# Optimization experiments

Hardware: AMD Instinct MI355X
Metric: run time of the kernel (lower is better)

## Reference

```python
import jax, jax.numpy as jnp
import numpy as np

VOCAB_P1 = 100001  # vocab_size + 1
EMB_DIM = 128
BATCH = 256
NNZ_Q = 2048
NNZ_D = 262144


def setup_inputs() -> dict:
    key = jax.random.key(0)
    ks = jax.random.split(key, 10)
    return {
        "q_rows": jax.random.randint(ks[0], (NNZ_Q,), 0, VOCAB_P1, dtype=jnp.int32),
        "q_cols": jax.random.randint(ks[1], (NNZ_Q,), 0, BATCH, dtype=jnp.int32),
        "q_vals": jax.random.uniform(ks[2], (NNZ_Q,), dtype=jnp.float32),
        "d_rows": jax.random.randint(ks[3], (NNZ_D,), 0, VOCAB_P1, dtype=jnp.int32),
        "d_cols": jax.random.randint(ks[4], (NNZ_D,), 0, BATCH, dtype=jnp.int32),
        "d_freqs": jax.random.uniform(ks[5], (NNZ_D,), dtype=jnp.float32),
        "emb": jax.random.normal(ks[6], (VOCAB_P1, EMB_DIM), dtype=jnp.float32) * 0.1,
        "W1": jax.random.normal(ks[7], (EMB_DIM, 100), dtype=jnp.float32) * (2.0 / EMB_DIM) ** 0.5,
        "b1": jnp.zeros((100,), dtype=jnp.float32),
        "W2": jax.random.normal(ks[8], (100, 1), dtype=jnp.float32) * (2.0 / 100) ** 0.5,
        "b2": jnp.ones((1,), dtype=jnp.float32),
        "mu": jnp.float32(2500.0),
        "batch_size": BATCH,
    }


def _scatter_dense(rows, cols, vals, batch_size):
    # tf.sparse.to_dense: dense [vocab+1, batch] with values at (row, col).
    # Indices are (assumed) unique, so add == set; add keeps it a clean scatter.
    return jnp.zeros((VOCAB_P1, batch_size), vals.dtype).at[rows, cols].add(vals)


def reference(q_rows, q_cols, q_vals, d_rows, d_cols, d_freqs,
              emb, W1, b1, W2, b2, mu, batch_size):
    # query bag-of-words dense tensor [V, B]
    q = _scatter_dense(q_rows, q_cols, q_vals, batch_size)

    # term discrimination value MLP on document terms (dropout disabled = eval mode)
    h = jax.nn.relu(emb[d_rows] @ W1 + b1)          # [nnz_d, 100]
    tdv = jax.nn.relu(h @ W2 + b2)[:, 0]            # [nnz_d]
    freq_tdv = tdv * d_freqs                        # [nnz_d]

    # weighted document term-frequency dense tensor [V, B]
    d = _scatter_dense(d_rows, d_cols, freq_tdv, batch_size)

    cfreq = jnp.sum(d, axis=1) / jnp.sum(d)                     # [V]
    smoothing = jnp.log(mu / (jnp.sum(d, axis=0) + mu))         # [B]
    dir_d = jnp.log1p(d / (1.0 + mu * cfreq[:, None])) + smoothing  # [V, B]
    rel = jnp.sum(q * dir_d, axis=0)                            # [B]
    return (rel, d)
```

## Files before the change

### kernel.cpp

```cpp
#include <hip/hip_runtime.h>
#include <stdint.h>

#define VOCAB_P1 100001
#define EMB_DIM  128
#define BATCH    256
#define NNZ_Q    2048
#define NNZ_D    262144

#define NPAD 112
#define ROWP 136
#define NGRP 6251
#define MBLK 1563
#define BINBLK 512

#define NBKT 3126
#define BCAP 192
#define CSC  64

#define WS_BCNT  0
#define WS_CS    12544
#define WS_TDV   78080
#define WS_RSUM  478096
#define WS_W1BF  878112
#define WS_BIN   908576

typedef __attribute__((ext_vector_type(8))) short  short8;
typedef __attribute__((ext_vector_type(4))) float  float4v;

__device__ __forceinline__ unsigned short f2bf(float f) {
    union { float f; unsigned u; } v; v.f = f;
    unsigned u = v.u;
    u += 0x7fffu + ((u >> 16) & 1u);
    return (unsigned short)(u >> 16);
}

__device__ __forceinline__ short8 cvt8(float4 a, float4 b) {
    short8 r;
    r[0] = (short)f2bf(a.x); r[1] = (short)f2bf(a.y);
    r[2] = (short)f2bf(a.z); r[3] = (short)f2bf(a.w);
    r[4] = (short)f2bf(b.x); r[5] = (short)f2bf(b.y);
    r[6] = (short)f2bf(b.z); r[7] = (short)f2bf(b.w);
    return r;
}

__global__ __launch_bounds__(256) void prep_kernel(
    float* __restrict__ rel, int* __restrict__ wsbase,
    int* __restrict__ w1bfi, const float* __restrict__ W1)
{
    int t = blockIdx.x * 256 + threadIdx.x;
    const int4 z = {0, 0, 0, 0};
    if (t < 4880) ((int4*)wsbase)[t] = z;
    else if (t < 4944) ((int4*)rel)[t - 4880] = z;
    for (int i = t; i < (NPAD * ROWP) / 2; i += 6144) {
        int p0 = 2 * i, p1 = 2 * i + 1;
        int j0 = p0 / ROWP, k0 = p0 - j0 * ROWP;
        int j1 = p1 / ROWP, k1 = p1 - j1 * ROWP;
        unsigned lo = (j0 < 100 && k0 < 128) ? f2bf(W1[k0 * 100 + j0]) : 0u;
        unsigned hi = (j1 < 100 && k1 < 128) ? f2bf(W1[k1 * 100 + j1]) : 0u;
        w1bfi[i] = (int)(lo | (hi << 16));
    }
}

__global__ __launch_bounds__(256) void mlp_bin_kernel(
    const float* __restrict__ emb, const float* __restrict__ b1,
    const float* __restrict__ W2, const float* __restrict__ b2,
    const short* __restrict__ w1bf, float* __restrict__ tdvtab,
    const int* __restrict__ d_rows, const int* __restrict__ d_cols,
    const float* __restrict__ d_freqs,
    int* __restrict__ bcnt, int2* __restrict__ binbuf)
{
    const int tid = threadIdx.x;

    if (blockIdx.x >= MBLK) {
        int g = (blockIdx.x - MBLK) * 256 + tid;
        int2   r2 = ((const int2*)d_rows)[g];
        int2   c2 = ((const int2*)d_cols)[g];
        float2 f2 = ((const float2*)d_freqs)[g];
        int bk0 = r2.x >> 5, bk1 = r2.y >> 5;
        int i0 = atomicAdd(&bcnt[bk0], 1);
        int i1 = atomicAdd(&bcnt[bk1], 1);
        if (i0 < BCAP)
            binbuf[bk0 * BCAP + i0] = make_int2(((r2.x & 31) << 8) | c2.x,
                                                __float_as_int(f2.x));
        if (i1 < BCAP)
            binbuf[bk1 * BCAP + i1] = make_int2(((r2.y & 31) << 8) | c2.y,
                                                __float_as_int(f2.y));
        return;
    }

    __shared__ __align__(16) short w1t[NPAD * ROWP];
    __shared__ float b1s[NPAD];
    __shared__ float w2s[NPAD];

    {
        const int4* src = (const int4*)w1bf;
        int4* dst = (int4*)w1t;
        #pragma unroll
        for (int k = 0; k < 8; ++k) {
            int idx = tid + k * 256;
            if (idx < (NPAD * ROWP * 2) / 16) dst[idx] = src[idx];
        }
    }
    if (tid < NPAD) {
        b1s[tid] = (tid < 100) ? b1[tid] : 0.f;
        w2s[tid] = (tid < 100) ? W2[tid] : 0.f;
    }
    __syncthreads();

    const int lane = tid & 63;
    const int w    = tid >> 6;
    const int col  = lane & 15;
    const int quad = lane >> 4;
    const float b2v = b2[0];

    const int grp = blockIdx.x * 4 + w;
    if (grp >= NGRP) return;

    int r  = grp * 16 + col;
    int rr = (r <= VOCAB_P1 - 1) ? r : (VOCAB_P1 - 1);
    const float* rp = emb + (size_t)rr * EMB_DIM + quad * 8;
    float4 u0 = *(const float4*)(rp);
    float4 u1 = *(const float4*)(rp + 4);
    float4 u2 = *(const float4*)(rp + 32);
    float4 u3 = *(const float4*)(rp + 36);
    float4 u4 = *(const float4*)(rp + 64);
    float4 u5 = *(const float4*)(rp + 68);
    float4 u6 = *(const float4*)(rp + 96);
    float4 u7 = *(const float4*)(rp + 100);
    short8 a0 = cvt8(u0, u1), a1 = cvt8(u2, u3);
    short8 a2 = cvt8(u4, u5), a3 = cvt8(u6, u7);

    float s0 = 0.f, s1 = 0.f, s2 = 0.f, s3 = 0.f;
    for (int jt = 0; jt < 7; ++jt) {
        const short* bp = &w1t[(jt * 16 + col) * ROWP + quad * 8];
        short8 bv0 = *(const short8*)(bp);
        short8 bv1 = *(const short8*)(bp + 32);
        short8 bv2 = *(const short8*)(bp + 64);
        short8 bv3 = *(const short8*)(bp + 96);

        float4v acc = {0.f, 0.f, 0.f, 0.f};
        acc = __builtin_amdgcn_mfma_f32_16x16x32_bf16(a0, bv0, acc, 0, 0, 0);
        acc = __builtin_amdgcn_mfma_f32_16x16x32_bf16(a1, bv1, acc, 0, 0, 0);
        acc = __builtin_amdgcn_mfma_f32_16x16x32_bf16(a2, bv2, acc, 0, 0, 0);
        acc = __builtin_amdgcn_mfma_f32_16x16x32_bf16(a3, bv3, acc, 0, 0, 0);

        float b1v = b1s[jt * 16 + col];
        float w2v = w2s[jt * 16 + col];
        float h;
        h = acc[0] + b1v; h = h > 0.f ? h : 0.f; s0 += h * w2v;
        h = acc[1] + b1v; h = h > 0.f ? h : 0.f; s1 += h * w2v;
        h = acc[2] + b1v; h = h > 0.f ? h : 0.f; s2 += h * w2v;
        h = acc[3] + b1v; h = h > 0.f ? h : 0.f; s3 += h * w2v;
    }
    for (int m = 1; m < 16; m <<= 1) {
        s0 += __shfl_xor(s0, m, 64);
        s1 += __shfl_xor(s1, m, 64);
        s2 += __shfl_xor(s2, m, 64);
        s3 += __shfl_xor(s3, m, 64);
    }
    if (col < 4) {
        float sv = (col == 0) ? s0 : (col == 1) ? s1 : (col == 2) ? s2 : s3;
        int row = grp * 16 + quad * 4 + col;
        if (row < VOCAB_P1) {
            float tdv = sv + b2v;
            tdvtab[row] = tdv > 0.f ? tdv : 0.f;
        }
    }
}

__global__ __launch_bounds__(256) void compose_kernel(
    const int* __restrict__ bcnt, const int2* __restrict__ binbuf,
    const float* __restrict__ tdvtab, float* __restrict__ dmat,
    float* __restrict__ rowsum, float* __restrict__ colsum2)
{
    __shared__ float tile[32 * 256];
    const int tid = threadIdx.x;
    const int blk = blockIdx.x;

    const float4 z = {0.f, 0.f, 0.f, 0.f};
    float4* t4 = (float4*)tile;
    #pragma unroll
    for (int k = 0; k < 8; ++k) t4[tid + k * 256] = z;
    __syncthreads();

    const int row0 = blk * 32;
    int cnt = bcnt[blk]; if (cnt > BCAP) cnt = BCAP;
    for (int i = tid; i < cnt; i += 256) {
        int2 e = binbuf[blk * BCAP + i];
        int rl = e.x >> 8, c = e.x & 255;
        float v = __int_as_float(e.y) * tdvtab[row0 + rl];
        atomicAdd(&tile[rl * 256 + c], v);
    }
    __syncthreads();

    int vrows = VOCAB_P1 - row0; if (vrows > 32) vrows = 32;

    float4* out4 = (float4*)(dmat + (size_t)row0 * BATCH);
    const int lim = vrows * 64;
    #pragma unroll
    for (int k = 0; k < 8; ++k) {
        int idx = tid + k * 256;
        if (idx < lim) out4[idx] = t4[idx];
    }

    {
        int rl = tid >> 3, seg = tid & 7;
        float s = 0.f;
        #pragma unroll
        for (int j = 0; j < 32; ++j)
            s += tile[rl * 256 + seg * 32 + ((j + tid) & 31)];
        s += __shfl_xor(s, 1, 64);
        s += __shfl_xor(s, 2, 64);
        s += __shfl_xor(s, 4, 64);
        if (seg == 0 && rl < vrows) rowsum[row0 + rl] = s;
    }

    {
        float cs = 0.f;
        #pragma unroll
        for (int r = 0; r < 32; ++r) cs += tile[r * 256 + tid];
        atomicAdd(&colsum2[(blk & (CSC - 1)) * BATCH + tid], cs);
    }
}

__global__ __launch_bounds__(256) void relv2_kernel(
    const int* __restrict__ q_rows, const int* __restrict__ q_cols,
    const float* __restrict__ q_vals, const float* __restrict__ dmat,
    const float* __restrict__ rowsum, const float* __restrict__ colsum2,
    const float* __restrict__ mu_p, float* __restrict__ rel)
{
    __shared__ float csT[BATCH];
    __shared__ float tot4[4];
    const int tid = threadIdx.x;

    float s = 0.f;
    #pragma unroll 8
    for (int k = 0; k < CSC; ++k) s += colsum2[k * BATCH + tid];
    csT[tid] = s;
    float p = s;
    for (int m = 1; m < 64; m <<= 1) p += __shfl_xor(p, m, 64);
    if ((tid & 63) == 0) tot4[tid >> 6] = p;
    __syncthreads();
    float total = tot4[0] + tot4[1] + tot4[2] + tot4[3];

    int e = blockIdx.x * 256 + tid;
    int v = q_rows[e], b = q_cols[e];
    float qv = q_vals[e];
    float mu = mu_p[0];
    float dval = dmat[(size_t)v * BATCH + b];
    float cf   = rowsum[v] / total;
    float dir  = log1pf(dval / (1.f + mu * cf)) + logf(mu / (csT[b] + mu));
    atomicAdd(&rel[b], qv * dir);
}

extern "C" void kernel_launch(void* const* d_in, const int* in_sizes, int n_in,
                              void* d_out, int out_size, void* d_ws, size_t ws_size,
                              hipStream_t stream)
{
    const int*   q_rows  = (const int*)d_in[0];
    const int*   q_cols  = (const int*)d_in[1];
    const float* q_vals  = (const float*)d_in[2];
    const int*   d_rows  = (const int*)d_in[3];
    const int*   d_cols  = (const int*)d_in[4];
    const float* d_freqs = (const float*)d_in[5];
    const float* emb     = (const float*)d_in[6];
    const float* W1      = (const float*)d_in[7];
    const float* b1      = (const float*)d_in[8];
    const float* W2      = (const float*)d_in[9];
    const float* b2      = (const float*)d_in[10];
    const float* mu      = (const float*)d_in[11];

    float* rel  = (float*)d_out;
    float* dmat = rel + BATCH;

    char*  ws      = (char*)d_ws;
    int*   bcnt    = (int*)(ws + WS_BCNT);
    float* colsum2 = (float*)(ws + WS_CS);
    float* tdvtab  = (float*)(ws + WS_TDV);
    float* rowsum  = (float*)(ws + WS_RSUM);
    short* w1bf    = (short*)(ws + WS_W1BF);
    int2*  binbuf  = (int2*)(ws + WS_BIN);

    prep_kernel<<<24, 256, 0, stream>>>(rel, (int*)ws, (int*)w1bf, W1);
    mlp_bin_kernel<<<MBLK + BINBLK, 256, 0, stream>>>(
        emb, b1, W2, b2, w1bf, tdvtab, d_rows, d_cols, d_freqs, bcnt, binbuf);
    compose_kernel<<<NBKT, 256, 0, stream>>>(
        bcnt, binbuf, tdvtab, dmat, rowsum, colsum2);
    relv2_kernel<<<NNZ_Q / 256, 256, 0, stream>>>(
        q_rows, q_cols, q_vals, dmat, rowsum, colsum2, mu, rel);
}
```

Before: 208.4 us.

## Fuse TDV MLP into compose kernel and move W1 conversion into binning

The per-row TDV MLP moves out of its own pass and into the compose kernel. Each 32-row bucket block now computes its 32 TDV values with MFMA into shared memory, and that shared buffer is aliased between the W1 tile and the accumulation tile. This removes the global TDV table round trip and one kernel boundary. W1 bf16 conversion moves into an extra block of the binning kernel, and workspace zeroing moves to hipMemsetAsync calls. In exchange, compose blocks now load W1 into LDS and run the MLP before scattering, which lengthens each block, and two memset operations are added.

```diff
diff --git a/kernel.cpp b/kernel.cpp
--- a/kernel.cpp
+++ b/kernel.cpp
@@ -10,7 +10,6 @@
 #define NPAD 112
 #define ROWP 136
 #define NGRP 6251
-#define MBLK 1563
 #define BINBLK 512
 
 #define NBKT 3126
@@ -19,10 +18,9 @@
 
 #define WS_BCNT  0
 #define WS_CS    12544
-#define WS_TDV   78080
-#define WS_RSUM  478096
-#define WS_W1BF  878112
-#define WS_BIN   908576
+#define WS_RSUM  78080
+#define WS_W1BF  478096
+#define WS_BIN   508560
 
 typedef __attribute__((ext_vector_type(8))) short  short8;
 typedef __attribute__((ext_vector_type(4))) float  float4v;
@@ -43,54 +41,59 @@
     return r;
 }
 
-__global__ __launch_bounds__(256) void prep_kernel(
-    float* __restrict__ rel, int* __restrict__ wsbase,
+__global__ __launch_bounds__(256) void bin_w1_kernel(
+    const int* __restrict__ d_rows, const int* __restrict__ d_cols,
+    const float* __restrict__ d_freqs,
+    int* __restrict__ bcnt, int2* __restrict__ binbuf,
     int* __restrict__ w1bfi, const float* __restrict__ W1)
 {
-    int t = blockIdx.x * 256 + threadIdx.x;
-    const int4 z = {0, 0, 0, 0};
-    if (t < 4880) ((int4*)wsbase)[t] = z;
-    else if (t < 4944) ((int4*)rel)[t - 4880] = z;
-    for (int i = t; i < (NPAD * ROWP) / 2; i += 6144) {
-        int p0 = 2 * i, p1 = 2 * i + 1;
-        int j0 = p0 / ROWP, k0 = p0 - j0 * ROWP;
-        int j1 = p1 / ROWP, k1 = p1 - j1 * ROWP;
-        unsigned lo = (j0 < 100 && k0 < 128) ? f2bf(W1[k0 * 100 + j0]) : 0u;
-        unsigned hi = (j1 < 100 && k1 < 128) ? f2bf(W1[k1 * 100 + j1]) : 0u;
-        w1bfi[i] = (int)(lo | (hi << 16));
-    }
-}
-
-__global__ __launch_bounds__(256) void mlp_bin_kernel(
+    const int tid = threadIdx.x;
+
+    if (blockIdx.x == BINBLK) {
+        for (int i = tid; i < (NPAD * ROWP) / 2; i += 256) {
+            int p0 = 2 * i, p1 = 2 * i + 1;
+            int j0 = p0 / ROWP, k0 = p0 - j0 * ROWP;
+            int j1 = p1 / ROWP, k1 = p1 - j1 * ROWP;
+            unsigned lo = (j0 < 100 && k0 < 128) ? f2bf(W1[k0 * 100 + j0]) : 0u;
+            unsigned hi = (j1 < 100 && k1 < 128) ? f2bf(W1[k1 * 100 + j1]) : 0u;
+            w1bfi[i] = (int)(lo | (hi << 16));
+        }
+        return;
+    }
+
+    int g = blockIdx.x * 256 + tid;
+    int2   r2 = ((const int2*)d_rows)[g];
+    int2   c2 = ((const int2*)d_cols)[g];
+    float2 f2 = ((const float2*)d_freqs)[g];
+    int bk0 = r2.x >> 5, bk1 = r2.y >> 5;
+    int i0 = atomicAdd(&bcnt[bk0], 1);
+    int i1 = atomicAdd(&bcnt[bk1], 1);
+    if (i0 < BCAP)
+        binbuf[bk0 * BCAP + i0] = make_int2(((r2.x & 31) << 8) | c2.x,
+                                            __float_as_int(f2.x));
+    if (i1 < BCAP)
+        binbuf[bk1 * BCAP + i1] = make_int2(((r2.y & 31) << 8) | c2.y,
+                                            __float_as_int(f2.y));
+}
+
+__global__ __launch_bounds__(256) void compose_kernel(
+    const int* __restrict__ bcnt, const int2* __restrict__ binbuf,
     const float* __restrict__ emb, const float* __restrict__ b1,
     const float* __restrict__ W2, const float* __restrict__ b2,
-    const short* __restrict__ w1bf, float* __restrict__ tdvtab,
-    const int* __restrict__ d_rows, const int* __restrict__ d_cols,
-    const float* __restrict__ d_freqs,
-    int* __restrict__ bcnt, int2* __restrict__ binbuf)
-{
-    const int tid = threadIdx.x;
-
-    if (blockIdx.x >= MBLK) {
-        int g = (blockIdx.x - MBLK) * 256 + tid;
-        int2   r2 = ((const int2*)d_rows)[g];
-        int2   c2 = ((const int2*)d_cols)[g];
-        float2 f2 = ((const float2*)d_freqs)[g];
-        int bk0 = r2.x >> 5, bk1 = r2.y >> 5;
-        int i0 = atomicAdd(&bcnt[bk0], 1);
-        int i1 = atomicAdd(&bcnt[bk1], 1);
-        if (i0 < BCAP)
-            binbuf[bk0 * BCAP + i0] = make_int2(((r2.x & 31) << 8) | c2.x,
-                                                __float_as_int(f2.x));
-        if (i1 < BCAP)
-            binbuf[bk1 * BCAP + i1] = make_int2(((r2.y & 31) << 8) | c2.y,
-                                                __float_as_int(f2.y));
-        return;
-    }
-
-    __shared__ __align__(16) short w1t[NPAD * ROWP];
+    const short* __restrict__ w1bf,
+    float* __restrict__ dmat, float* __restrict__ rowsum,
+    float* __restrict__ colsum2)
+{
+    __shared__ __align__(16) char uu[32 * 256 * 4];
+    short* w1t  = (short*)uu;
+    float* tile = (float*)uu;
     __shared__ float b1s[NPAD];
     __shared__ float w2s[NPAD];
+    __shared__ float tdv32[32];
+
+    const int tid = threadIdx.x;
+    const int blk = blockIdx.x;
+    const int row0 = blk * 32;
 
     {
         const int4* src = (const int4*)w1bf;
@@ -105,102 +108,102 @@
         b1s[tid] = (tid < 100) ? b1[tid] : 0.f;
         w2s[tid] = (tid < 100) ? W2[tid] : 0.f;
     }
-    __syncthreads();
-
-    const int lane = tid & 63;
-    const int w    = tid >> 6;
-    const int col  = lane & 15;
-    const int quad = lane >> 4;
-    const float b2v = b2[0];
-
-    const int grp = blockIdx.x * 4 + w;
-    if (grp >= NGRP) return;
-
-    int r  = grp * 16 + col;
-    int rr = (r <= VOCAB_P1 - 1) ? r : (VOCAB_P1 - 1);
-    const float* rp = emb + (size_t)rr * EMB_DIM + quad * 8;
-    float4 u0 = *(const float4*)(rp);
-    float4 u1 = *(const float4*)(rp + 4);
-    float4 u2 = *(const float4*)(rp + 32);
-    float4 u3 = *(const float4*)(rp + 36);
-    float4 u4 = *(const float4*)(rp + 64);
-    float4 u5 = *(const float4*)(rp + 68);
-    float4 u6 = *(const float4*)(rp + 96);
-    float4 u7 = *(const float4*)(rp + 100);
-    short8 a0 = cvt8(u0, u1), a1 = cvt8(u2, u3);
-    short8 a2 = cvt8(u4, u5), a3 = cvt8(u6, u7);
-
-    float s0 = 0.f, s1 = 0.f, s2 = 0.f, s3 = 0.f;
-    for (int jt = 0; jt < 7; ++jt) {
-        const short* bp = &w1t[(jt * 16 + col) * ROWP + quad * 8];
-        short8 bv0 = *(const short8*)(bp);
-        short8 bv1 = *(const short8*)(bp + 32);
-        short8 bv2 = *(const short8*)(bp + 64);
-        short8 bv3 = *(const short8*)(bp + 96);
-
-        float4v acc = {0.f, 0.f, 0.f, 0.f};
-        acc = __builtin_amdgcn_mfma_f32_16x16x32_bf16(a0, bv0, acc, 0, 0, 0);
-        acc = __builtin_amdgcn_mfma_f32_16x16x32_bf16(a1, bv1, acc, 0, 0, 0);
-        acc = __builtin_amdgcn_mfma_f32_16x16x32_bf16(a2, bv2, acc, 0, 0, 0);
-        acc = __builtin_amdgcn_mfma_f32_16x16x32_bf16(a3, bv3, acc, 0, 0, 0);
-
-        float b1v = b1s[jt * 16 + col];
-        float w2v = w2s[jt * 16 + col];
-        float h;
-        h = acc[0] + b1v; h = h > 0.f ? h : 0.f; s0 += h * w2v;
-        h = acc[1] + b1v; h = h > 0.f ? h : 0.f; s1 += h * w2v;
-        h = acc[2] + b1v; h = h > 0.f ? h : 0.f; s2 += h * w2v;
-        h = acc[3] + b1v; h = h > 0.f ? h : 0.f; s3 += h * w2v;
-    }
-    for (int m = 1; m < 16; m <<= 1) {
-        s0 += __shfl_xor(s0, m, 64);
-        s1 += __shfl_xor(s1, m, 64);
-        s2 += __shfl_xor(s2, m, 64);
-        s3 += __shfl_xor(s3, m, 64);
-    }
-    if (col < 4) {
-        float sv = (col == 0) ? s0 : (col == 1) ? s1 : (col == 2) ? s2 : s3;
-        int row = grp * 16 + quad * 4 + col;
-        if (row < VOCAB_P1) {
-            float tdv = sv + b2v;
-            tdvtab[row] = tdv > 0.f ? tdv : 0.f;
-        }
-    }
-}
-
-__global__ __launch_bounds__(256) void compose_kernel(
-    const int* __restrict__ bcnt, const int2* __restrict__ binbuf,
-    const float* __restrict__ tdvtab, float* __restrict__ dmat,
-    float* __restrict__ rowsum, float* __restrict__ colsum2)
-{
-    __shared__ float tile[32 * 256];
-    const int tid = threadIdx.x;
-    const int blk = blockIdx.x;
-
-    const float4 z = {0.f, 0.f, 0.f, 0.f};
-    float4* t4 = (float4*)tile;
-    #pragma unroll
-    for (int k = 0; k < 8; ++k) t4[tid + k * 256] = z;
-    __syncthreads();
-
-    const int row0 = blk * 32;
+
     int cnt = bcnt[blk]; if (cnt > BCAP) cnt = BCAP;
-    for (int i = tid; i < cnt; i += 256) {
-        int2 e = binbuf[blk * BCAP + i];
+    int bi = (tid < cnt) ? tid : 0;
+    int2 e = binbuf[blk * BCAP + bi];
+
+    __syncthreads();
+
+    {
+        const int lane = tid & 63;
+        const int w    = tid >> 6;
+        const int col  = lane & 15;
+        const int quad = lane >> 4;
+        const int grp  = blk * 2 + w;
+
+        if (w < 2 && grp < NGRP) {
+            const float b2v = b2[0];
+            int r  = grp * 16 + col;
+            int rr = (r <= VOCAB_P1 - 1) ? r : (VOCAB_P1 - 1);
+            const float* rp = emb + (size_t)rr * EMB_DIM + quad * 8;
+            float4 u0 = *(const float4*)(rp);
+            float4 u1 = *(const float4*)(rp + 4);
+            float4 u2 = *(const float4*)(rp + 32);
+            float4 u3 = *(const float4*)(rp + 36);
+            float4 u4 = *(const float4*)(rp + 64);
+            float4 u5 = *(const float4*)(rp + 68);
+            float4 u6 = *(const float4*)(rp + 96);
+            float4 u7 = *(const float4*)(rp + 100);
+            short8 a0 = cvt8(u0, u1), a1 = cvt8(u2, u3);
+            short8 a2 = cvt8(u4, u5), a3 = cvt8(u6, u7);
+
+            float s0 = 0.f, s1 = 0.f, s2 = 0.f, s3 = 0.f;
+            for (int jt = 0; jt < 7; ++jt) {
+                const short* bp = &w1t[(jt * 16 + col) * ROWP + quad * 8];
+                short8 bv0 = *(const short8*)(bp);
+                short8 bv1 = *(const short8*)(bp + 32);
+                short8 bv2 = *(const short8*)(bp + 64);
+                short8 bv3 = *(const short8*)(bp + 96);
+
+                float4v acc = {0.f, 0.f, 0.f, 0.f};
+                acc = __builtin_amdgcn_mfma_f32_16x16x32_bf16(a0, bv0, acc, 0, 0, 0);
+                acc = __builtin_amdgcn_mfma_f32_16x16x32_bf16(a1, bv1, acc, 0, 0, 0);
+                acc = __builtin_amdgcn_mfma_f32_16x16x32_bf16(a2, bv2, acc, 0, 0, 0);
+                acc = __builtin_amdgcn_mfma_f32_16x16x32_bf16(a3, bv3, acc, 0, 0, 0);
+
+                float b1v = b1s[jt * 16 + col];
+                float w2v = w2s[jt * 16 + col];
+                float h;
+                h = acc[0] + b1v; h = h > 0.f ? h : 0.f; s0 += h * w2v;
+                h = acc[1] + b1v; h = h > 0.f ? h : 0.f; s1 += h * w2v;
+                h = acc[2] + b1v; h = h > 0.f ? h : 0.f; s2 += h * w2v;
+                h = acc[3] + b1v; h = h > 0.f ? h : 0.f; s3 += h * w2v;
+            }
+            for (int m = 1; m < 16; m <<= 1) {
+                s0 += __shfl_xor(s0, m, 64);
+                s1 += __shfl_xor(s1, m, 64);
+                s2 += __shfl_xor(s2, m, 64);
+                s3 += __shfl_xor(s3, m, 64);
+            }
+            if (col < 4) {
+                float sv = (col == 0) ? s0 : (col == 1) ? s1 : (col == 2) ? s2 : s3;
+                int row = grp * 16 + quad * 4 + col;
+                if (row < VOCAB_P1) {
+                    float tdv = sv + b2v;
+                    tdv32[w * 16 + quad * 4 + col] = tdv > 0.f ? tdv : 0.f;
+                }
+            }
+        }
+    }
+    __syncthreads();
+
+    {
+        const float4 z = {0.f, 0.f, 0.f, 0.f};
+        float4* t4 = (float4*)tile;
+        #pragma unroll
+        for (int k = 0; k < 8; ++k) t4[tid + k * 256] = z;
+    }
+    __syncthreads();
+
+    if (tid < cnt) {
         int rl = e.x >> 8, c = e.x & 255;
-        float v = __int_as_float(e.y) * tdvtab[row0 + rl];
+        float v = __int_as_float(e.y) * tdv32[rl];
         atomicAdd(&tile[rl * 256 + c], v);
     }
     __syncthreads();
 
     int vrows = VOCAB_P1 - row0; if (vrows > 32) vrows = 32;
 
-    float4* out4 = (float4*)(dmat + (size_t)row0 * BATCH);
-    const int lim = vrows * 64;
-    #pragma unroll
-    for (int k = 0; k < 8; ++k) {
-        int idx = tid + k * 256;
-        if (idx < lim) out4[idx] = t4[idx];
+    {
+        float4* out4 = (float4*)(dmat + (size_t)row0 * BATCH);
+        float4* t4 = (float4*)tile;
+        const int lim = vrows * 64;
+        #pragma unroll
+        for (int k = 0; k < 8; ++k) {
+            int idx = tid + k * 256;
+            if (idx < lim) out4[idx] = t4[idx];
+        }
     }
 
     {
@@ -276,16 +279,17 @@
     char*  ws      = (char*)d_ws;
     int*   bcnt    = (int*)(ws + WS_BCNT);
     float* colsum2 = (float*)(ws + WS_CS);
-    float* tdvtab  = (float*)(ws + WS_TDV);
     float* rowsum  = (float*)(ws + WS_RSUM);
     short* w1bf    = (short*)(ws + WS_W1BF);
     int2*  binbuf  = (int2*)(ws + WS_BIN);
 
-    prep_kernel<<<24, 256, 0, stream>>>(rel, (int*)ws, (int*)w1bf, W1);
-    mlp_bin_kernel<<<MBLK + BINBLK, 256, 0, stream>>>(
-        emb, b1, W2, b2, w1bf, tdvtab, d_rows, d_cols, d_freqs, bcnt, binbuf);
+    hipMemsetAsync(ws, 0, WS_RSUM, stream);
+    hipMemsetAsync(rel, 0, BATCH * sizeof(float), stream);
+
+    bin_w1_kernel<<<BINBLK + 1, 256, 0, stream>>>(
+        d_rows, d_cols, d_freqs, bcnt, binbuf, (int*)w1bf, W1);
     compose_kernel<<<NBKT, 256, 0, stream>>>(
-        bcnt, binbuf, tdvtab, dmat, rowsum, colsum2);
+        bcnt, binbuf, emb, b1, W2, b2, w1bf, dmat, rowsum, colsum2);
     relv2_kernel<<<NNZ_Q / 256, 256, 0, stream>>>(
         q_rows, q_cols, q_vals, dmat, rowsum, colsum2, mu, rel);
 }
```

Result: slower. 226.8 us (+8.8%).

## Fold prep kernel into MLP/bin kernel and fuse row/col sums into scatter

Applied to the files above, without the earlier changes.

Removes the separate prep kernel. Workspace zeroing moves to hipMemsetAsync and zeroing of rel moves to one extra block of the MLP/bin kernel. Each MLP block now converts W1 to bf16 and transposes it into shared memory itself, so the W1 conversion is repeated in all 1563 blocks. In compose_kernel, row and column sums are accumulated with shared-memory atomics during the scatter, which replaces the separate tile reduction passes, and the tdv values are staged in shared memory. Bin blocks are reordered to launch first. The scatter loop is reduced to a single pass (tid<cnt), which is only correct because BCAP (192) is smaller than 256.

```diff
diff --git a/kernel.cpp b/kernel.cpp
--- a/kernel.cpp
+++ b/kernel.cpp
@@ -10,8 +10,8 @@
 #define NPAD 112
 #define ROWP 136
 #define NGRP 6251
+#define BINBLK 512
 #define MBLK 1563
-#define BINBLK 512
 
 #define NBKT 3126
 #define BCAP 192
@@ -21,8 +21,7 @@
 #define WS_CS    12544
 #define WS_TDV   78080
 #define WS_RSUM  478096
-#define WS_W1BF  878112
-#define WS_BIN   908576
+#define WS_BIN   878112
 
 typedef __attribute__((ext_vector_type(8))) short  short8;
 typedef __attribute__((ext_vector_type(4))) float  float4v;
@@ -43,36 +42,19 @@
     return r;
 }
 
-__global__ __launch_bounds__(256) void prep_kernel(
-    float* __restrict__ rel, int* __restrict__ wsbase,
-    int* __restrict__ w1bfi, const float* __restrict__ W1)
-{
-    int t = blockIdx.x * 256 + threadIdx.x;
-    const int4 z = {0, 0, 0, 0};
-    if (t < 4880) ((int4*)wsbase)[t] = z;
-    else if (t < 4944) ((int4*)rel)[t - 4880] = z;
-    for (int i = t; i < (NPAD * ROWP) / 2; i += 6144) {
-        int p0 = 2 * i, p1 = 2 * i + 1;
-        int j0 = p0 / ROWP, k0 = p0 - j0 * ROWP;
-        int j1 = p1 / ROWP, k1 = p1 - j1 * ROWP;
-        unsigned lo = (j0 < 100 && k0 < 128) ? f2bf(W1[k0 * 100 + j0]) : 0u;
-        unsigned hi = (j1 < 100 && k1 < 128) ? f2bf(W1[k1 * 100 + j1]) : 0u;
-        w1bfi[i] = (int)(lo | (hi << 16));
-    }
-}
-
 __global__ __launch_bounds__(256) void mlp_bin_kernel(
-    const float* __restrict__ emb, const float* __restrict__ b1,
-    const float* __restrict__ W2, const float* __restrict__ b2,
-    const short* __restrict__ w1bf, float* __restrict__ tdvtab,
     const int* __restrict__ d_rows, const int* __restrict__ d_cols,
     const float* __restrict__ d_freqs,
-    int* __restrict__ bcnt, int2* __restrict__ binbuf)
+    int* __restrict__ bcnt, int2* __restrict__ binbuf,
+    const float* __restrict__ emb, const float* __restrict__ W1,
+    const float* __restrict__ b1, const float* __restrict__ W2,
+    const float* __restrict__ b2, float* __restrict__ tdvtab,
+    float* __restrict__ rel)
 {
     const int tid = threadIdx.x;
 
-    if (blockIdx.x >= MBLK) {
-        int g = (blockIdx.x - MBLK) * 256 + tid;
+    if (blockIdx.x < BINBLK) {
+        int g = blockIdx.x * 256 + tid;
         int2   r2 = ((const int2*)d_rows)[g];
         int2   c2 = ((const int2*)d_cols)[g];
         float2 f2 = ((const float2*)d_freqs)[g];
@@ -87,19 +69,21 @@
                                                 __float_as_int(f2.y));
         return;
     }
+    if (blockIdx.x == BINBLK) {
+        rel[tid] = 0.f;
+        return;
+    }
 
     __shared__ __align__(16) short w1t[NPAD * ROWP];
     __shared__ float b1s[NPAD];
     __shared__ float w2s[NPAD];
 
-    {
-        const int4* src = (const int4*)w1bf;
-        int4* dst = (int4*)w1t;
-        #pragma unroll
-        for (int k = 0; k < 8; ++k) {
-            int idx = tid + k * 256;
-            if (idx < (NPAD * ROWP * 2) / 16) dst[idx] = src[idx];
-        }
+    int* w1i = (int*)w1t;
+    for (int i = tid; i < NPAD * ROWP / 2; i += 256) w1i[i] = 0;
+    __syncthreads();
+    for (int f = tid; f < EMB_DIM * 100; f += 256) {
+        int k = f / 100, j = f - k * 100;
+        w1t[j * ROWP + k] = (short)f2bf(W1[f]);
     }
     if (tid < NPAD) {
         b1s[tid] = (tid < 100) ? b1[tid] : 0.f;
@@ -113,7 +97,7 @@
     const int quad = lane >> 4;
     const float b2v = b2[0];
 
-    const int grp = blockIdx.x * 4 + w;
+    const int grp = (blockIdx.x - (BINBLK + 1)) * 4 + w;
     if (grp >= NGRP) return;
 
     int r  = grp * 16 + col;
@@ -174,53 +158,50 @@
     float* __restrict__ rowsum, float* __restrict__ colsum2)
 {
     __shared__ float tile[32 * 256];
+    __shared__ float rs[32];
+    __shared__ float cs[BATCH];
+    __shared__ float tdvs[32];
     const int tid = threadIdx.x;
     const int blk = blockIdx.x;
+    const int row0 = blk * 32;
 
     const float4 z = {0.f, 0.f, 0.f, 0.f};
     float4* t4 = (float4*)tile;
     #pragma unroll
     for (int k = 0; k < 8; ++k) t4[tid + k * 256] = z;
-    __syncthreads();
-
-    const int row0 = blk * 32;
+    if (tid < 32) {
+        rs[tid] = 0.f;
+        int r = row0 + tid;
+        tdvs[tid] = (r < VOCAB_P1) ? tdvtab[r] : 0.f;
+    }
+    cs[tid] = 0.f;
     int cnt = bcnt[blk]; if (cnt > BCAP) cnt = BCAP;
-    for (int i = tid; i < cnt; i += 256) {
-        int2 e = binbuf[blk * BCAP + i];
+    __syncthreads();
+
+    if (tid < cnt) {
+        int2 e = binbuf[blk * BCAP + tid];
         int rl = e.x >> 8, c = e.x & 255;
-        float v = __int_as_float(e.y) * tdvtab[row0 + rl];
+        float v = __int_as_float(e.y) * tdvs[rl];
         atomicAdd(&tile[rl * 256 + c], v);
+        atomicAdd(&rs[rl], v);
+        atomicAdd(&cs[c], v);
     }
     __syncthreads();
 
     int vrows = VOCAB_P1 - row0; if (vrows > 32) vrows = 32;
 
-    float4* out4 = (float4*)(dmat + (size_t)row0 * BATCH);
-    const int lim = vrows * 64;
-    #pragma unroll
-    for (int k = 0; k < 8; ++k) {
-        int idx = tid + k * 256;
-        if (idx < lim) out4[idx] = t4[idx];
-    }
-
     {
-        int rl = tid >> 3, seg = tid & 7;
-        float s = 0.f;
+        float4* out4 = (float4*)(dmat + (size_t)row0 * BATCH);
+        const int lim = vrows * 64;
         #pragma unroll
-        for (int j = 0; j < 32; ++j)
-            s += tile[rl * 256 + seg * 32 + ((j + tid) & 31)];
-        s += __shfl_xor(s, 1, 64);
-        s += __shfl_xor(s, 2, 64);
-        s += __shfl_xor(s, 4, 64);
-        if (seg == 0 && rl < vrows) rowsum[row0 + rl] = s;
-    }
-
-    {
-        float cs = 0.f;
-        #pragma unroll
-        for (int r = 0; r < 32; ++r) cs += tile[r * 256 + tid];
-        atomicAdd(&colsum2[(blk & (CSC - 1)) * BATCH + tid], cs);
-    }
+        for (int k = 0; k < 8; ++k) {
+            int idx = tid + k * 256;
+            if (idx < lim) out4[idx] = t4[idx];
+        }
+    }
+
+    if (tid < vrows) rowsum[row0 + tid] = rs[tid];
+    atomicAdd(&colsum2[(blk & (CSC - 1)) * BATCH + tid], cs[tid]);
 }
 
 __global__ __launch_bounds__(256) void relv2_kernel(
@@ -278,12 +259,13 @@
     float* colsum2 = (float*)(ws + WS_CS);
     float* tdvtab  = (float*)(ws + WS_TDV);
     float* rowsum  = (float*)(ws + WS_RSUM);
-    short* w1bf    = (short*)(ws + WS_W1BF);
     int2*  binbuf  = (int2*)(ws + WS_BIN);
 
-    prep_kernel<<<24, 256, 0, stream>>>(rel, (int*)ws, (int*)w1bf, W1);
-    mlp_bin_kernel<<<MBLK + BINBLK, 256, 0, stream>>>(
-        emb, b1, W2, b2, w1bf, tdvtab, d_rows, d_cols, d_freqs, bcnt, binbuf);
+    hipMemsetAsync(ws, 0, WS_TDV, stream);
+
+    mlp_bin_kernel<<<BINBLK + 1 + MBLK, 256, 0, stream>>>(
+        d_rows, d_cols, d_freqs, bcnt, binbuf,
+        emb, W1, b1, W2, b2, tdvtab, rel);
     compose_kernel<<<NBKT, 256, 0, stream>>>(
         bcnt, binbuf, tdvtab, dmat, rowsum, colsum2);
     relv2_kernel<<<NNZ_Q / 256, 256, 0, stream>>>(
```

After: 209.9 us. About the same (+0.7%).
